# Kernel tuning notes

Measured on AMD Instinct MI355X. Metric: run time of the kernel, lower is better.

## Reference

```python
import jax, jax.numpy as jnp
import numpy as np

B, N, D, NS, H, ITERS = 16, 2048, 128, 8, 128, 3
EPS = 1e-8


def _ln(x, g, b):
    m = jnp.mean(x, -1, keepdims=True)
    v = jnp.mean((x - m) ** 2, -1, keepdims=True)
    return (x - m) * jax.lax.rsqrt(v + 1e-5) * g + b


def _gru(x, h, Wih, Whh, bih, bhh):
    # PyTorch GRUCell math
    gi = x @ Wih.T + bih
    gh = h @ Whh.T + bhh
    ir, iz, inn = jnp.split(gi, 3, -1)
    hr, hz, hn = jnp.split(gh, 3, -1)
    r = jax.nn.sigmoid(ir + hr)
    z = jax.nn.sigmoid(iz + hz)
    n = jnp.tanh(inn + r * hn)
    return (1.0 - z) * n + z * h


def setup_inputs() -> dict:
    key = jax.random.key(0)
    ks = jax.random.split(key, 16)

    def lin(k, out_d, in_d):
        lim = 1.0 / np.sqrt(in_d)
        return jax.random.uniform(k, (out_d, in_d), jnp.float32, -lim, lim)

    return {
        "inputs": jax.random.normal(ks[0], (B, N, D), jnp.float32),
        "init_noise": jax.random.normal(ks[1], (B, NS, 2 * D), jnp.float32),
        "slots_mu": jax.random.normal(ks[2], (1, 1, 2 * D), jnp.float32),
        "slots_logsigma": jax.random.normal(ks[3], (1, 1, 2 * D), jnp.float32) * 0.08,  # ~xavier scale
        "Wq": lin(ks[4], D, D),
        "Wk": lin(ks[5], D, D),
        "gru_Wih": lin(ks[6], 3 * D, D),
        "gru_Whh": lin(ks[7], 3 * D, D),
        "gru_bih": jnp.zeros((3 * D,), jnp.float32),
        "gru_bhh": jnp.zeros((3 * D,), jnp.float32),
        "mlp_mu_W1": lin(ks[8], H, D),
        "mlp_mu_b1": jnp.zeros((H,), jnp.float32),
        "mlp_mu_W2": lin(ks[9], D, H),
        "mlp_mu_b2": jnp.zeros((D,), jnp.float32),
        "ln_in_g": jnp.ones((D,), jnp.float32),
        "ln_in_b": jnp.zeros((D,), jnp.float32),
        "ln_slots_g": jnp.ones((2 * D,), jnp.float32),
        "ln_slots_b": jnp.zeros((2 * D,), jnp.float32),
        "ln_mu_g": jnp.ones((D,), jnp.float32),
        "ln_mu_b": jnp.zeros((D,), jnp.float32),
        "mlp_out_W1": lin(ks[10], 2 * H, 2 * D),
        "mlp_out_b1": jnp.zeros((2 * H,), jnp.float32),
        "mlp_out_W2": lin(ks[11], D, 2 * H),
        "mlp_out_b2": jnp.zeros((D,), jnp.float32),
    }


def _forward(inputs, init_noise, slots_mu, slots_logsigma, Wq, Wk,
             gru_Wih, gru_Whh, gru_bih, gru_bhh,
             mlp_mu_W1, mlp_mu_b1, mlp_mu_W2, mlp_mu_b2,
             ln_in_g, ln_in_b, ln_slots_g, ln_slots_b, ln_mu_g, ln_mu_b,
             mlp_out_W1, mlp_out_b1, mlp_out_W2, mlp_out_b2):
    x = _ln(inputs, ln_in_g, ln_in_b)                      # (B,N,D)
    k = x @ Wk.T
    v = k                                                  # original uses to_k for both k and v
    slots = slots_mu + jnp.exp(slots_logsigma) * init_noise  # (B,NS,2D)
    pi_cl = jnp.full((B, NS, 1), 1.0 / NS, inputs.dtype)

    def step(slots, pi_cl):
        s = _ln(slots, ln_slots_g, ln_slots_b)
        mu_s, ls_s = jnp.split(s, 2, -1)                   # (B,NS,D) each
        q_mu = mu_s @ Wq.T
        q_ls = ls_s @ Wq.T
        inv_var = jnp.exp(-2.0 * q_ls)                     # 1 / exp(q_logsigma)^2
        diff = k[:, None, :, :] - q_mu[:, :, None, :]      # (B,NS,N,D)
        dots = jnp.einsum('bind,bid->bin', diff * diff, inv_var)
        dots_exp = (jnp.exp(-dots) + EPS) * pi_cl          # (B,NS,N)
        gammas = dots_exp / dots_exp.sum(1, keepdims=True)
        attn = gammas / gammas.sum(-1, keepdims=True)
        upd = jnp.einsum('bjd,bij->bid', v, attn)          # (B,NS,D)
        upd = _gru(upd.reshape(-1, D), mu_s.reshape(-1, D),
                   gru_Wih, gru_Whh, gru_bih, gru_bhh).reshape(B, NS, D)
        h = _ln(upd, ln_mu_g, ln_mu_b)
        upd = upd + (jax.nn.relu(h @ mlp_mu_W1.T + mlp_mu_b1) @ mlp_mu_W2.T + mlp_mu_b2)
        diff2 = v[:, None, :, :] - upd[:, :, None, :]      # (B,NS,N,D)
        upd_ls = 0.5 * jnp.log(jnp.einsum('bind,bin->bid', diff2 * diff2 + EPS, attn))
        slots_new = jnp.concatenate([upd, upd_ls], -1)
        pi_new = gammas.sum(-1, keepdims=True)
        pi_new = pi_new / pi_new.shape[2]                  # shape[2]==1: faithful no-op from original
        return slots_new, pi_new

    for _ in range(ITERS):
        slots, pi_cl = step(slots, pi_cl)
    slots, pi_cl = step(jax.lax.stop_gradient(slots), pi_cl)
    h = jax.nn.relu(slots @ mlp_out_W1.T + mlp_out_b1)
    return h @ mlp_out_W2.T + mlp_out_b2                   # (B,NS,D)


def reference(inputs, init_noise, slots_mu, slots_logsigma, Wq, Wk,
              gru_Wih, gru_Whh, gru_bih, gru_bhh,
              mlp_mu_W1, mlp_mu_b1, mlp_mu_W2, mlp_mu_b2,
              ln_in_g, ln_in_b, ln_slots_g, ln_slots_b, ln_mu_g, ln_mu_b,
              mlp_out_W1, mlp_out_b1, mlp_out_W2, mlp_out_b2):
    return _forward(inputs, init_noise, slots_mu, slots_logsigma, Wq, Wk,
                    gru_Wih, gru_Whh, gru_bih, gru_bhh,
                    mlp_mu_W1, mlp_mu_b1, mlp_mu_W2, mlp_mu_b2,
                    ln_in_g, ln_in_b, ln_slots_g, ln_slots_b, ln_mu_g, ln_mu_b,
                    mlp_out_W1, mlp_out_b1, mlp_out_W2, mlp_out_b2)
```

## Files before the change

### kernel.cpp

```cpp
#include <hip/hip_runtime.h>

#define EPS_ 1e-8f

constexpr int OFF_K     = 0;
constexpr int OFF_WQT   = 4194304;
constexpr int OFF_WKT   = OFF_WQT  + 16384;
constexpr int OFF_WIHT  = OFF_WKT  + 16384;
constexpr int OFF_WHHT  = OFF_WIHT + 49152;
constexpr int OFF_WM1T  = OFF_WHHT + 49152;
constexpr int OFF_WM2T  = OFF_WM1T + 16384;
constexpr int OFF_WO1T  = OFF_WM2T + 16384;
constexpr int OFF_WO2T  = OFF_WO1T + 65536;
constexpr int OFF_SLOTS = OFF_WO2T + 32768;
constexpr int OFF_PI    = OFF_SLOTS+ 32768;
constexpr int OFF_MUS   = OFF_PI   + 128;
constexpr int OFF_QMU   = OFF_MUS  + 16384;
constexpr int OFF_IVAR  = OFF_QMU  + 16384;
constexpr int OFF_UN    = OFF_IVAR + 16384;
constexpr int OFF_S2    = OFF_UN   + 262144;
constexpr int OFF_DEN   = OFF_S2   + 262144;

__global__ __launch_bounds__(256) void init_kernel(
    const float* __restrict__ Wq,  const float* __restrict__ Wk,
    const float* __restrict__ Wih, const float* __restrict__ Whh,
    const float* __restrict__ Wm1, const float* __restrict__ Wm2,
    const float* __restrict__ Wo1, const float* __restrict__ Wo2,
    const float* __restrict__ smu, const float* __restrict__ sls,
    const float* __restrict__ noise, float* __restrict__ ws) {
  int idx = blockIdx.x * 256 + threadIdx.x;
  if (idx < 16384) { int j = idx >> 7, d = idx & 127; ws[OFF_WQT + d*128 + j] = Wq[idx]; return; }
  idx -= 16384;
  if (idx < 16384) { int j = idx >> 7, d = idx & 127; ws[OFF_WKT + d*128 + j] = Wk[idx]; return; }
  idx -= 16384;
  if (idx < 49152) { int j = idx >> 7, d = idx & 127; ws[OFF_WIHT + d*384 + j] = Wih[idx]; return; }
  idx -= 49152;
  if (idx < 49152) { int j = idx >> 7, d = idx & 127; ws[OFF_WHHT + d*384 + j] = Whh[idx]; return; }
  idx -= 49152;
  if (idx < 16384) { int j = idx >> 7, d = idx & 127; ws[OFF_WM1T + d*128 + j] = Wm1[idx]; return; }
  idx -= 16384;
  if (idx < 16384) { int j = idx >> 7, d = idx & 127; ws[OFF_WM2T + d*128 + j] = Wm2[idx]; return; }
  idx -= 16384;
  if (idx < 65536) { int j = idx >> 8, d = idx & 255; ws[OFF_WO1T + d*256 + j] = Wo1[idx]; return; }
  idx -= 65536;
  if (idx < 32768) { int j = idx >> 8, m = idx & 255; ws[OFF_WO2T + m*128 + j] = Wo2[idx]; return; }
  idx -= 32768;
  if (idx < 32768) { int c = idx & 255; ws[OFF_SLOTS + idx] = smu[c] + expf(sls[c]) * noise[idx]; return; }
  idx -= 32768;
  if (idx < 128) { ws[OFF_PI + idx] = 0.125f; }
}

__global__ __launch_bounds__(256) void k_kernel(
    const float* __restrict__ xin, const float* __restrict__ g, const float* __restrict__ bb,
    const float* __restrict__ WkT, float* __restrict__ kout) {
  __shared__ float xs[16][128];
  __shared__ float2 red[16][16];
  __shared__ float mrow[16], srow[16];
  int t = threadIdx.x;
  int base = blockIdx.x * 2048;
  const float4* in4 = (const float4*)(xin + base);
  for (int f = t; f < 512; f += 256) {
    float4 v = in4[f];
    *(float4*)&xs[f >> 5][(f & 31) * 4] = v;
  }
  __syncthreads();
  {
    int row = t >> 4, l = t & 15;
    float s = 0.f, ss = 0.f;
    #pragma unroll
    for (int d = 0; d < 128; d += 16) { float v = xs[row][d + l]; s += v; ss = fmaf(v, v, ss); }
    red[row][l] = make_float2(s, ss);
  }
  __syncthreads();
  if (t < 16) {
    float s = 0.f, ss = 0.f;
    #pragma unroll
    for (int l = 0; l < 16; ++l) { float2 p = red[t][l]; s += p.x; ss += p.y; }
    float m = s * (1.0f/128.0f);
    float var = ss * (1.0f/128.0f) - m * m;
    mrow[t] = m;
    srow[t] = rsqrtf(var + 1e-5f);
  }
  __syncthreads();
  for (int f = t; f < 2048; f += 256) {
    int row = f >> 7, d = f & 127;
    xs[row][d] = (xs[row][d] - mrow[row]) * srow[row] * g[d] + bb[d];
  }
  __syncthreads();
  int j = t & 127, half = t >> 7;
  float acc[8] = {0,0,0,0,0,0,0,0};
  const int r0 = half * 8;
  #pragma unroll 4
  for (int d = 0; d < 128; ++d) {
    float w = WkT[d * 128 + j];
    #pragma unroll
    for (int r = 0; r < 8; ++r) acc[r] = fmaf(w, xs[r0 + r][d], acc[r]);
  }
  #pragma unroll
  for (int r = 0; r < 8; ++r) kout[base + (r0 + r) * 128 + j] = acc[r];
}

__global__ __launch_bounds__(256) void s1_kernel(
    const float* __restrict__ slots, const float* __restrict__ g, const float* __restrict__ bb,
    const float* __restrict__ WqT, float* __restrict__ mus, float* __restrict__ qmu,
    float* __restrict__ ivar) {
  __shared__ float sl[256];
  __shared__ float2 wr[4];
  int t = threadIdx.x, bi = blockIdx.x;
  float v = slots[bi * 256 + t];
  float s = v, ss = v * v;
  #pragma unroll
  for (int o = 32; o > 0; o >>= 1) { s += __shfl_down(s, o); ss += __shfl_down(ss, o); }
  if ((t & 63) == 0) wr[t >> 6] = make_float2(s, ss);
  __syncthreads();
  float fs  = wr[0].x + wr[1].x + wr[2].x + wr[3].x;
  float fss = wr[0].y + wr[1].y + wr[2].y + wr[3].y;
  float m   = fs * (1.0f/256.0f);
  float var = fss * (1.0f/256.0f) - m * m;
  float isr = rsqrtf(var + 1e-5f);
  float sn  = (v - m) * isr * g[t] + bb[t];
  sl[t] = sn;
  __syncthreads();
  if (t < 128) {
    float acc = 0.f;
    #pragma unroll 4
    for (int d = 0; d < 128; ++d) acc = fmaf(sl[d], WqT[d * 128 + t], acc);
    qmu[bi * 128 + t] = acc;
    mus[bi * 128 + t] = sn;
  } else {
    int jj = t - 128;
    float acc = 0.f;
    #pragma unroll 4
    for (int d = 0; d < 128; ++d) acc = fmaf(sl[128 + d], WqT[d * 128 + jj], acc);
    ivar[bi * 128 + jj] = expf(-2.0f * acc);
  }
}

__global__ __launch_bounds__(1024) void s2_kernel(
    const float* __restrict__ kmat, const float* __restrict__ qmu,
    const float* __restrict__ ivar, const float* __restrict__ pi,
    float* __restrict__ wun, float* __restrict__ ws2, float* __restrict__ wden) {
  __shared__ float kc[128][132];
  __shared__ float qs[8 * 132];
  __shared__ float ivs[8 * 132];
  __shared__ float es[8 * 132];
  __shared__ float gam[128 * 12];
  __shared__ float recip[128];
  __shared__ float pis[8];
  __shared__ float pU[4][8][128];
  __shared__ float pS[4][8][128];
  __shared__ float pd[8][8];
  int t = threadIdx.x;
  int chunk = blockIdx.x, b = blockIdx.y;
  if (t < 8) pis[t] = pi[b * 8 + t];
  { int ii = t >> 7, dd = t & 127;
    qs[ii * 132 + dd]  = qmu[b * 1024 + t];
    ivs[ii * 132 + dd] = ivar[b * 1024 + t]; }
  const float4* k4 = (const float4*)(kmat + (b * 2048 + chunk * 128) * 128);
  for (int f = t; f < 4096; f += 1024)
    *(float4*)&kc[f >> 5][(f & 31) * 4] = k4[f];
  __syncthreads();
  if (t < 512) {
    int gsl = t & 7, n0 = (t >> 3) << 1;
    float acc0 = 0.f, acc1 = 0.f;
    const float* qrow = qs + gsl * 132;
    const float* irow = ivs + gsl * 132;
    const float* k0r  = &kc[n0][0];
    const float* k1r  = &kc[n0 + 1][0];
    #pragma unroll 4
    for (int dq = 0; dq < 32; ++dq) {
      float4 qv = *(const float4*)(qrow + dq * 4);
      float4 iv = *(const float4*)(irow + dq * 4);
      float4 k0 = *(const float4*)(k0r + dq * 4);
      float4 k1 = *(const float4*)(k1r + dq * 4);
      float e;
      e = k0.x - qv.x; acc0 = fmaf(e * e, iv.x, acc0);
      e = k0.y - qv.y; acc0 = fmaf(e * e, iv.y, acc0);
      e = k0.z - qv.z; acc0 = fmaf(e * e, iv.z, acc0);
      e = k0.w - qv.w; acc0 = fmaf(e * e, iv.w, acc0);
      e = k1.x - qv.x; acc1 = fmaf(e * e, iv.x, acc1);
      e = k1.y - qv.y; acc1 = fmaf(e * e, iv.y, acc1);
      e = k1.z - qv.z; acc1 = fmaf(e * e, iv.z, acc1);
      e = k1.w - qv.w; acc1 = fmaf(e * e, iv.w, acc1);
    }
    es[gsl * 132 + n0]     = (expf(-acc0) + EPS_) * pis[gsl];
    es[gsl * 132 + n0 + 1] = (expf(-acc1) + EPS_) * pis[gsl];
  }
  __syncthreads();
  if (t < 128) {
    float ssum = 0.f;
    #pragma unroll
    for (int g2 = 0; g2 < 8; ++g2) ssum += es[g2 * 132 + t];
    recip[t] = 1.0f / ssum;
  }
  __syncthreads();
  { int ii = t >> 7, n = t & 127;
    gam[n * 12 + ii] = es[ii * 132 + n] * recip[n]; }
  __syncthreads();
  if (t < 512) {
    int grp = t >> 7, dd = t & 127;
    float un[8] = {0,0,0,0,0,0,0,0};
    float s2[8] = {0,0,0,0,0,0,0,0};
    #pragma unroll 2
    for (int n = grp * 32; n < grp * 32 + 32; ++n) {
      float kk  = kc[n][dd];
      float kk2 = kk * kk;
      float4 g0 = *(const float4*)&gam[n * 12];
      float4 g1 = *(const float4*)&gam[n * 12 + 4];
      un[0] = fmaf(g0.x, kk, un[0]); s2[0] = fmaf(g0.x, kk2, s2[0]);
      un[1] = fmaf(g0.y, kk, un[1]); s2[1] = fmaf(g0.y, kk2, s2[1]);
      un[2] = fmaf(g0.z, kk, un[2]); s2[2] = fmaf(g0.z, kk2, s2[2]);
      un[3] = fmaf(g0.w, kk, un[3]); s2[3] = fmaf(g0.w, kk2, s2[3]);
      un[4] = fmaf(g1.x, kk, un[4]); s2[4] = fmaf(g1.x, kk2, s2[4]);
      un[5] = fmaf(g1.y, kk, un[5]); s2[5] = fmaf(g1.y, kk2, s2[5]);
      un[6] = fmaf(g1.z, kk, un[6]); s2[6] = fmaf(g1.z, kk2, s2[6]);
      un[7] = fmaf(g1.w, kk, un[7]); s2[7] = fmaf(g1.w, kk2, s2[7]);
    }
    #pragma unroll
    for (int ii = 0; ii < 8; ++ii) { pU[grp][ii][dd] = un[ii]; pS[grp][ii][dd] = s2[ii]; }
  } else if (t < 576) {
    int ii = (t - 512) & 7, sub = (t - 512) >> 3;
    float dsum = 0.f;
    for (int n = sub * 16; n < sub * 16 + 16; ++n) dsum += gam[n * 12 + ii];
    pd[sub][ii] = dsum;
  }
  __syncthreads();
  { int ii = t >> 7, dd = t & 127;
    int pbase = ((b * 16 + chunk) * 8 + ii) * 128 + dd;
    wun[pbase] = pU[0][ii][dd] + pU[1][ii][dd] + pU[2][ii][dd] + pU[3][ii][dd];
    ws2[pbase] = pS[0][ii][dd] + pS[1][ii][dd] + pS[2][ii][dd] + pS[3][ii][dd]; }
  if (t < 8) {
    float s = 0.f;
    #pragma unroll
    for (int sub = 0; sub < 8; ++sub) s += pd[sub][t];
    wden[(b * 16 + chunk) * 8 + t] = s;
  }
}

__global__ __launch_bounds__(512) void s3_kernel(
    const float* __restrict__ wun, const float* __restrict__ ws2, const float* __restrict__ wden,
    const float* __restrict__ WihT, const float* __restrict__ WhhT,
    const float* __restrict__ bih,  const float* __restrict__ bhh,
    const float* __restrict__ Wm1T, const float* __restrict__ bm1,
    const float* __restrict__ Wm2T, const float* __restrict__ bm2,
    const float* __restrict__ gmu,  const float* __restrict__ bmu,
    float* __restrict__ slots, float* __restrict__ pi,
    int do_s1,
    const float* __restrict__ gs, const float* __restrict__ bs,
    const float* __restrict__ WqT,
    float* __restrict__ mus, float* __restrict__ qmu, float* __restrict__ ivar,
    const float* __restrict__ Wo1T, const float* __restrict__ bo1,
    const float* __restrict__ Wo2T, const float* __restrict__ bo2,
    float* __restrict__ out) {
  int t = threadIdx.x, bi = blockIdx.x;
  int d = t & 127, q = t >> 7;
  int b = bi >> 3, i = bi & 7;
  __shared__ float redU[4][128], redS[4][128];
  __shared__ float dred[16];
  __shared__ float xs[128], hs[128];
  __shared__ float gacc[4][6][128];
  __shared__ float ga[6][128];
  __shared__ float grus[128], hl[128], m1s[128];
  __shared__ float macc[4][128];
  __shared__ float2 wr2[2];
  __shared__ float uarr[256];
  float unp = 0.f, s2p = 0.f;
  #pragma unroll
  for (int c = q * 4; c < q * 4 + 4; ++c) {
    int po = ((b * 16 + c) * 8 + i) * 128 + d;
    unp += wun[po]; s2p += ws2[po];
  }
  redU[q][d] = unp; redS[q][d] = s2p;
  if (t < 16) dred[t] = wden[(b * 16 + t) * 8 + i];
  if (q == 1) hs[d] = mus[bi * 128 + d];
  __syncthreads();
  float den = 0.f;
  #pragma unroll
  for (int c = 0; c < 16; ++c) den += dred[c];
  float un  = redU[0][d] + redU[1][d] + redU[2][d] + redU[3][d];
  float s2v = redS[0][d] + redS[1][d] + redS[2][d] + redS[3][d];
  if (q == 0) xs[d] = un / den;
  __syncthreads();
  {
    float a0 = 0, a1 = 0, a2 = 0, a3 = 0, a4 = 0, a5 = 0;
    #pragma unroll 4
    for (int dd = q * 32; dd < q * 32 + 32; ++dd) {
      float xv = xs[dd], hv = hs[dd];
      const float* wi = &WihT[dd * 384 + d];
      const float* wh = &WhhT[dd * 384 + d];
      a0 = fmaf(xv, wi[0],   a0);
      a1 = fmaf(xv, wi[128], a1);
      a2 = fmaf(xv, wi[256], a2);
      a3 = fmaf(hv, wh[0],   a3);
      a4 = fmaf(hv, wh[128], a4);
      a5 = fmaf(hv, wh[256], a5);
    }
    gacc[q][0][d] = a0; gacc[q][1][d] = a1; gacc[q][2][d] = a2;
    gacc[q][3][d] = a3; gacc[q][4][d] = a4; gacc[q][5][d] = a5;
  }
  __syncthreads();
  for (int f = t; f < 768; f += 512) {
    int j = f >> 7, dd = f & 127;
    ga[j][dd] = gacc[0][j][dd] + gacc[1][j][dd] + gacc[2][j][dd] + gacc[3][j][dd];
  }
  __syncthreads();
  float gru = 0.f;
  if (q == 0) {
    float ir = ga[0][d] + bih[d], iz = ga[1][d] + bih[128 + d], inn = ga[2][d] + bih[256 + d];
    float hr = ga[3][d] + bhh[d], hz = ga[4][d] + bhh[128 + d], hn  = ga[5][d] + bhh[256 + d];
    float r  = 1.0f / (1.0f + expf(-(ir + hr)));
    float z  = 1.0f / (1.0f + expf(-(iz + hz)));
    float nn = tanhf(inn + r * hn);
    gru = (1.0f - z) * nn + z * hs[d];
    grus[d] = gru;
    float s = gru, ssq = gru * gru;
    #pragma unroll
    for (int o = 32; o > 0; o >>= 1) { s += __shfl_down(s, o); ssq += __shfl_down(ssq, o); }
    if ((d & 63) == 0) wr2[d >> 6] = make_float2(s, ssq);
  }
  __syncthreads();
  if (q == 0) {
    float fs = wr2[0].x + wr2[1].x, fss = wr2[0].y + wr2[1].y;
    float mean = fs * (1.0f/128.0f);
    float var  = fss * (1.0f/128.0f) - mean * mean;
    hl[d] = (gru - mean) * rsqrtf(var + 1e-5f) * gmu[d] + bmu[d];
  }
  __syncthreads();
  {
    float m1p = 0.f;
    #pragma unroll 4
    for (int dd = q * 32; dd < q * 32 + 32; ++dd)
      m1p = fmaf(hl[dd], Wm1T[dd * 128 + d], m1p);
    macc[q][d] = m1p;
  }
  __syncthreads();
  if (q == 0) m1s[d] = fmaxf(macc[0][d] + macc[1][d] + macc[2][d] + macc[3][d] + bm1[d], 0.f);
  __syncthreads();
  {
    float m2p = 0.f;
    #pragma unroll 4
    for (int dd = q * 32; dd < q * 32 + 32; ++dd)
      m2p = fmaf(m1s[dd], Wm2T[dd * 128 + d], m2p);
    macc[q][d] = m2p;
  }
  __syncthreads();
  if (q == 0) {
    float u = grus[d] + macc[0][d] + macc[1][d] + macc[2][d] + macc[3][d] + bm2[d];
    float val = (s2v - 2.0f * u * un + u * u * den) / den;
    float ls = 0.5f * logf(fmaxf(val, 0.0f) + EPS_);
    slots[bi * 256 + d]       = u;
    slots[bi * 256 + 128 + d] = ls;
    uarr[d] = u; uarr[128 + d] = ls;
    if (d == 0) pi[bi] = den;
  }
  __syncthreads();
  if (do_s1) {
    __shared__ float2 wr4[4];
    __shared__ float sln[256];
    __shared__ float qacc[2][2][128];
    if (t < 256) {
      float v = uarr[t];
      float s = v, ssq = v * v;
      #pragma unroll
      for (int o = 32; o > 0; o >>= 1) { s += __shfl_down(s, o); ssq += __shfl_down(ssq, o); }
      if ((t & 63) == 0) wr4[t >> 6] = make_float2(s, ssq);
    }
    __syncthreads();
    if (t < 256) {
      float fs  = wr4[0].x + wr4[1].x + wr4[2].x + wr4[3].x;
      float fss = wr4[0].y + wr4[1].y + wr4[2].y + wr4[3].y;
      float m   = fs * (1.0f/256.0f);
      float var = fss * (1.0f/256.0f) - m * m;
      sln[t] = (uarr[t] - m) * rsqrtf(var + 1e-5f) * gs[t] + bs[t];
    }
    __syncthreads();
    {
      int h2 = t >> 8, qq = (t >> 7) & 1, d2 = t & 127;
      const float* src = sln + h2 * 128;
      float acc = 0.f;
      #pragma unroll 4
      for (int dd = qq * 64; dd < qq * 64 + 64; ++dd)
        acc = fmaf(src[dd], WqT[dd * 128 + d2], acc);
      qacc[h2][qq][d2] = acc;
    }
    __syncthreads();
    if (t < 128) {
      qmu[bi * 128 + t] = qacc[0][0][t] + qacc[0][1][t];
      mus[bi * 128 + t] = sln[t];
    } else if (t < 256) {
      int dd2 = t - 128;
      ivar[bi * 128 + dd2] = expf(-2.0f * (qacc[1][0][dd2] + qacc[1][1][dd2]));
    }
  } else {
    __shared__ float oacc[2][256];
    __shared__ float hh[256];
    {
      int o = t & 255, qq = t >> 8;
      float acc = 0.f;
      #pragma unroll 4
      for (int dd = qq * 128; dd < qq * 128 + 128; ++dd)
        acc = fmaf(uarr[dd], Wo1T[dd * 256 + o], acc);
      oacc[qq][o] = acc;
    }
    __syncthreads();
    if (t < 256) hh[t] = fmaxf(oacc[0][t] + oacc[1][t] + bo1[t], 0.f);
    __syncthreads();
    {
      int o2 = t & 127, q4 = t >> 7;
      float acc2 = 0.f;
      #pragma unroll 4
      for (int dd = q4 * 64; dd < q4 * 64 + 64; ++dd)
        acc2 = fmaf(hh[dd], Wo2T[dd * 128 + o2], acc2);
      macc[q4][o2] = acc2;
    }
    __syncthreads();
    if (t < 128) out[bi * 128 + t] = macc[0][t] + macc[1][t] + macc[2][t] + macc[3][t] + bo2[t];
  }
}

extern "C" void kernel_launch(void* const* d_in, const int* in_sizes, int n_in,
                              void* d_out, int out_size, void* d_ws, size_t ws_size,
                              hipStream_t stream) {
  const float* inputs = (const float*)d_in[0];
  const float* noise  = (const float*)d_in[1];
  const float* smu    = (const float*)d_in[2];
  const float* sls    = (const float*)d_in[3];
  const float* Wq     = (const float*)d_in[4];
  const float* Wk     = (const float*)d_in[5];
  const float* Wih    = (const float*)d_in[6];
  const float* Whh    = (const float*)d_in[7];
  const float* bih    = (const float*)d_in[8];
  const float* bhh    = (const float*)d_in[9];
  const float* Wm1    = (const float*)d_in[10];
  const float* bm1    = (const float*)d_in[11];
  const float* Wm2    = (const float*)d_in[12];
  const float* bm2    = (const float*)d_in[13];
  const float* gin    = (const float*)d_in[14];
  const float* bin    = (const float*)d_in[15];
  const float* gsl    = (const float*)d_in[16];
  const float* bsl    = (const float*)d_in[17];
  const float* gmu    = (const float*)d_in[18];
  const float* bmu    = (const float*)d_in[19];
  const float* Wo1    = (const float*)d_in[20];
  const float* bo1    = (const float*)d_in[21];
  const float* Wo2    = (const float*)d_in[22];
  const float* bo2    = (const float*)d_in[23];

  float* ws    = (float*)d_ws;
  float* kbuf  = ws + OFF_K;
  float* WqT   = ws + OFF_WQT;
  float* WkT   = ws + OFF_WKT;
  float* WihT  = ws + OFF_WIHT;
  float* WhhT  = ws + OFF_WHHT;
  float* Wm1T  = ws + OFF_WM1T;
  float* Wm2T  = ws + OFF_WM2T;
  float* Wo1T  = ws + OFF_WO1T;
  float* Wo2T  = ws + OFF_WO2T;
  float* slots = ws + OFF_SLOTS;
  float* pibuf = ws + OFF_PI;
  float* mus   = ws + OFF_MUS;
  float* qmu   = ws + OFF_QMU;
  float* ivar  = ws + OFF_IVAR;
  float* wun   = ws + OFF_UN;
  float* ws2   = ws + OFF_S2;
  float* wden  = ws + OFF_DEN;

  hipLaunchKernelGGL(init_kernel, dim3(1153), dim3(256), 0, stream,
                     Wq, Wk, Wih, Whh, Wm1, Wm2, Wo1, Wo2, smu, sls, noise, ws);
  hipLaunchKernelGGL(k_kernel, dim3(2048), dim3(256), 0, stream,
                     inputs, gin, bin, WkT, kbuf);
  hipLaunchKernelGGL(s1_kernel, dim3(128), dim3(256), 0, stream,
                     slots, gsl, bsl, WqT, mus, qmu, ivar);
  for (int s = 0; s < 4; ++s) {
    hipLaunchKernelGGL(s2_kernel, dim3(16, 16), dim3(1024), 0, stream,
                       kbuf, qmu, ivar, pibuf, wun, ws2, wden);
    hipLaunchKernelGGL(s3_kernel, dim3(128), dim3(512), 0, stream,
                       wun, ws2, wden, WihT, WhhT, bih, bhh,
                       Wm1T, bm1, Wm2T, bm2, gmu, bmu, slots, pibuf,
                       (s < 3) ? 1 : 0, gsl, bsl, WqT, mus, qmu, ivar,
                       Wo1T, bo1, Wo2T, bo2, (float*)d_out);
  }
}
```

Baseline: 168.4 us.

## Retile key projection with shared-memory weights and rework s2 distance-stage mapping

The key-projection kernel now processes 64 rows per block, stages the full WkT matrix in shared memory, and has each thread compute 32 outputs for one row with vectorized float4 stores. This cuts the grid from 2048 to 512 blocks and is meant to reduce repeated global weight reads. In s2, the K chunk is stored with an XOR-swizzled float4 layout to avoid bank conflicts. All 1024 threads now compute the distance scores, split over two halves of the feature dimension and combined afterward, which costs an extra shared buffer and barrier. Shared-memory use per block rises sharply in both kernels, which may reduce occupancy.

Measured after the change: 181.4 us. 1.08x slower.

```diff
diff --git a/kernel.cpp b/kernel.cpp
--- a/kernel.cpp
+++ b/kernel.cpp
@@ -52,51 +52,68 @@
 __global__ __launch_bounds__(256) void k_kernel(
     const float* __restrict__ xin, const float* __restrict__ g, const float* __restrict__ bb,
     const float* __restrict__ WkT, float* __restrict__ kout) {
-  __shared__ float xs[16][128];
-  __shared__ float2 red[16][16];
-  __shared__ float mrow[16], srow[16];
+  __shared__ float xs[64][129];
+  __shared__ float4 wt4[128 * 32];
+  __shared__ float2 red2[64][4];
+  __shared__ float mrow[64], srow[64];
   int t = threadIdx.x;
-  int base = blockIdx.x * 2048;
+  long long base = (long long)blockIdx.x * 64 * 128;
   const float4* in4 = (const float4*)(xin + base);
-  for (int f = t; f < 512; f += 256) {
+  for (int f = t; f < 2048; f += 256) {
     float4 v = in4[f];
-    *(float4*)&xs[f >> 5][(f & 31) * 4] = v;
-  }
-  __syncthreads();
-  {
-    int row = t >> 4, l = t & 15;
+    int r = f >> 5, gg = (f & 31) * 4;
+    xs[r][gg] = v.x; xs[r][gg + 1] = v.y; xs[r][gg + 2] = v.z; xs[r][gg + 3] = v.w;
+  }
+  const float4* w4 = (const float4*)WkT;
+  for (int f = t; f < 4096; f += 256) wt4[f] = w4[f];
+  __syncthreads();
+  {
+    int r = t >> 2, qq = t & 3;
     float s = 0.f, ss = 0.f;
-    #pragma unroll
-    for (int d = 0; d < 128; d += 16) { float v = xs[row][d + l]; s += v; ss = fmaf(v, v, ss); }
-    red[row][l] = make_float2(s, ss);
-  }
-  __syncthreads();
-  if (t < 16) {
+    #pragma unroll 8
+    for (int u = 0; u < 32; ++u) { float v = xs[r][qq * 32 + u]; s += v; ss = fmaf(v, v, ss); }
+    red2[r][qq] = make_float2(s, ss);
+  }
+  __syncthreads();
+  if (t < 64) {
     float s = 0.f, ss = 0.f;
     #pragma unroll
-    for (int l = 0; l < 16; ++l) { float2 p = red[t][l]; s += p.x; ss += p.y; }
-    float m = s * (1.0f/128.0f);
-    float var = ss * (1.0f/128.0f) - m * m;
-    mrow[t] = m;
-    srow[t] = rsqrtf(var + 1e-5f);
-  }
-  __syncthreads();
-  for (int f = t; f < 2048; f += 256) {
-    int row = f >> 7, d = f & 127;
-    xs[row][d] = (xs[row][d] - mrow[row]) * srow[row] * g[d] + bb[d];
-  }
-  __syncthreads();
-  int j = t & 127, half = t >> 7;
-  float acc[8] = {0,0,0,0,0,0,0,0};
-  const int r0 = half * 8;
-  #pragma unroll 4
+    for (int qq = 0; qq < 4; ++qq) { float2 p = red2[t][qq]; s += p.x; ss += p.y; }
+    float m = s * (1.0f / 128.0f);
+    float var = ss * (1.0f / 128.0f) - m * m;
+    mrow[t] = m; srow[t] = rsqrtf(var + 1e-5f);
+  }
+  __syncthreads();
+  {
+    int r = t >> 2, qq = t & 3;
+    float m = mrow[r], is = srow[r];
+    #pragma unroll 8
+    for (int u = 0; u < 32; ++u) {
+      int d = qq * 32 + u;
+      xs[r][d] = (xs[r][d] - m) * is * g[d] + bb[d];
+    }
+  }
+  __syncthreads();
+  int r = t & 63, jg = t >> 6;
+  float acc[32];
+  #pragma unroll
+  for (int i = 0; i < 32; ++i) acc[i] = 0.f;
+  #pragma unroll 2
   for (int d = 0; d < 128; ++d) {
-    float w = WkT[d * 128 + j];
-    #pragma unroll
-    for (int r = 0; r < 8; ++r) acc[r] = fmaf(w, xs[r0 + r][d], acc[r]);
-  }
+    float xv = xs[r][d];
+    #pragma unroll
+    for (int i = 0; i < 8; ++i) {
+      float4 wv = wt4[d * 32 + jg * 8 + i];
+      acc[i * 4 + 0] = fmaf(xv, wv.x, acc[i * 4 + 0]);
+      acc[i * 4 + 1] = fmaf(xv, wv.y, acc[i * 4 + 1]);
+      acc[i * 4 + 2] = fmaf(xv, wv.z, acc[i * 4 + 2]);
+      acc[i * 4 + 3] = fmaf(xv, wv.w, acc[i * 4 + 3]);
+    }
+  }
+  float* orow = kout + base + (long long)r * 128 + jg * 32;
   #pragma unroll
-  for (int r = 0; r < 8; ++r) kout[base + (r0 + r) * 128 + j] = acc[r];
+  for (int i = 0; i < 8; ++i)
+    *(float4*)(orow + i * 4) = make_float4(acc[i*4], acc[i*4+1], acc[i*4+2], acc[i*4+3]);
 }
 
 __global__ __launch_bounds__(256) void s1_kernel(
@@ -139,11 +156,12 @@
     const float* __restrict__ kmat, const float* __restrict__ qmu,
     const float* __restrict__ ivar, const float* __restrict__ pi,
     float* __restrict__ wun, float* __restrict__ ws2, float* __restrict__ wden) {
-  __shared__ float kc[128][132];
-  __shared__ float qs[8 * 132];
-  __shared__ float ivs[8 * 132];
-  __shared__ float es[8 * 132];
-  __shared__ float gam[128 * 12];
+  __shared__ float4 kc4[128 * 32];
+  __shared__ float4 qs4[8 * 32];
+  __shared__ float4 ivs4[8 * 32];
+  __shared__ float esp[2][8][128];
+  __shared__ float es_[8][128];
+  __shared__ float gam_[128][8];
   __shared__ float recip[128];
   __shared__ float pis[8];
   __shared__ float pU[4][8][128];
@@ -152,60 +170,72 @@
   int t = threadIdx.x;
   int chunk = blockIdx.x, b = blockIdx.y;
   if (t < 8) pis[t] = pi[b * 8 + t];
-  { int ii = t >> 7, dd = t & 127;
-    qs[ii * 132 + dd]  = qmu[b * 1024 + t];
-    ivs[ii * 132 + dd] = ivar[b * 1024 + t]; }
-  const float4* k4 = (const float4*)(kmat + (b * 2048 + chunk * 128) * 128);
-  for (int f = t; f < 4096; f += 1024)
-    *(float4*)&kc[f >> 5][(f & 31) * 4] = k4[f];
-  __syncthreads();
-  if (t < 512) {
-    int gsl = t & 7, n0 = (t >> 3) << 1;
+  if (t < 256) {
+    qs4[t]  = ((const float4*)qmu)[b * 256 + t];
+    ivs4[t] = ((const float4*)ivar)[b * 256 + t];
+  }
+  const float4* k4 = (const float4*)(kmat + (long long)(b * 2048 + chunk * 128) * 128);
+  for (int f = t; f < 4096; f += 1024) {
+    int n = f >> 5, gg = f & 31;
+    kc4[n * 32 + (gg ^ (n & 31))] = k4[f];
+  }
+  __syncthreads();
+  {
+    int w = t >> 6, lane = t & 63;
+    int sp = w & 3, nh = (w >> 2) & 1, dh = w >> 3;
+    int s0 = sp * 2, s1 = s0 + 1;
+    int n = nh * 64 + lane;
+    int nx = n & 31;
+    const float4* kr = kc4 + n * 32;
     float acc0 = 0.f, acc1 = 0.f;
-    const float* qrow = qs + gsl * 132;
-    const float* irow = ivs + gsl * 132;
-    const float* k0r  = &kc[n0][0];
-    const float* k1r  = &kc[n0 + 1][0];
-    #pragma unroll 4
-    for (int dq = 0; dq < 32; ++dq) {
-      float4 qv = *(const float4*)(qrow + dq * 4);
-      float4 iv = *(const float4*)(irow + dq * 4);
-      float4 k0 = *(const float4*)(k0r + dq * 4);
-      float4 k1 = *(const float4*)(k1r + dq * 4);
+    #pragma unroll
+    for (int gi = 0; gi < 16; ++gi) {
+      int gg = dh * 16 + gi;
+      float4 kv = kr[gg ^ nx];
+      float4 q0 = qs4[s0 * 32 + gg], i0 = ivs4[s0 * 32 + gg];
+      float4 q1 = qs4[s1 * 32 + gg], i1 = ivs4[s1 * 32 + gg];
       float e;
-      e = k0.x - qv.x; acc0 = fmaf(e * e, iv.x, acc0);
-      e = k0.y - qv.y; acc0 = fmaf(e * e, iv.y, acc0);
-      e = k0.z - qv.z; acc0 = fmaf(e * e, iv.z, acc0);
-      e = k0.w - qv.w; acc0 = fmaf(e * e, iv.w, acc0);
-      e = k1.x - qv.x; acc1 = fmaf(e * e, iv.x, acc1);
-      e = k1.y - qv.y; acc1 = fmaf(e * e, iv.y, acc1);
-      e = k1.z - qv.z; acc1 = fmaf(e * e, iv.z, acc1);
-      e = k1.w - qv.w; acc1 = fmaf(e * e, iv.w, acc1);
-    }
-    es[gsl * 132 + n0]     = (expf(-acc0) + EPS_) * pis[gsl];
-    es[gsl * 132 + n0 + 1] = (expf(-acc1) + EPS_) * pis[gsl];
+      e = kv.x - q0.x; acc0 = fmaf(e * e, i0.x, acc0);
+      e = kv.y - q0.y; acc0 = fmaf(e * e, i0.y, acc0);
+      e = kv.z - q0.z; acc0 = fmaf(e * e, i0.z, acc0);
+      e = kv.w - q0.w; acc0 = fmaf(e * e, i0.w, acc0);
+      e = kv.x - q1.x; acc1 = fmaf(e * e, i1.x, acc1);
+      e = kv.y - q1.y; acc1 = fmaf(e * e, i1.y, acc1);
+      e = kv.z - q1.z; acc1 = fmaf(e * e, i1.z, acc1);
+      e = kv.w - q1.w; acc1 = fmaf(e * e, i1.w, acc1);
+    }
+    esp[dh][s0][n] = acc0;
+    esp[dh][s1][n] = acc1;
+  }
+  __syncthreads();
+  {
+    int s = t >> 7, n = t & 127;
+    float dots = esp[0][s][n] + esp[1][s][n];
+    es_[s][n] = (expf(-dots) + EPS_) * pis[s];
   }
   __syncthreads();
   if (t < 128) {
     float ssum = 0.f;
     #pragma unroll
-    for (int g2 = 0; g2 < 8; ++g2) ssum += es[g2 * 132 + t];
+    for (int s = 0; s < 8; ++s) ssum += es_[s][t];
     recip[t] = 1.0f / ssum;
   }
   __syncthreads();
-  { int ii = t >> 7, n = t & 127;
-    gam[n * 12 + ii] = es[ii * 132 + n] * recip[n]; }
+  { int s = t >> 7, n = t & 127;
+    gam_[n][s] = es_[s][n] * recip[n]; }
   __syncthreads();
   if (t < 512) {
     int grp = t >> 7, dd = t & 127;
+    const float* kcf = (const float*)kc4;
     float un[8] = {0,0,0,0,0,0,0,0};
     float s2[8] = {0,0,0,0,0,0,0,0};
+    int gbase = dd >> 2, elem = dd & 3;
     #pragma unroll 2
     for (int n = grp * 32; n < grp * 32 + 32; ++n) {
-      float kk  = kc[n][dd];
+      float kk  = kcf[n * 128 + 4 * (gbase ^ (n & 31)) + elem];
       float kk2 = kk * kk;
-      float4 g0 = *(const float4*)&gam[n * 12];
-      float4 g1 = *(const float4*)&gam[n * 12 + 4];
+      float4 g0 = *(const float4*)&gam_[n][0];
+      float4 g1 = *(const float4*)&gam_[n][4];
       un[0] = fmaf(g0.x, kk, un[0]); s2[0] = fmaf(g0.x, kk2, s2[0]);
       un[1] = fmaf(g0.y, kk, un[1]); s2[1] = fmaf(g0.y, kk2, s2[1]);
       un[2] = fmaf(g0.z, kk, un[2]); s2[2] = fmaf(g0.z, kk2, s2[2]);
@@ -216,18 +246,18 @@
       un[7] = fmaf(g1.w, kk, un[7]); s2[7] = fmaf(g1.w, kk2, s2[7]);
     }
     #pragma unroll
-    for (int ii = 0; ii < 8; ++ii) { pU[grp][ii][dd] = un[ii]; pS[grp][ii][dd] = s2[ii]; }
+    for (int i = 0; i < 8; ++i) { pU[grp][i][dd] = un[i]; pS[grp][i][dd] = s2[i]; }
   } else if (t < 576) {
-    int ii = (t - 512) & 7, sub = (t - 512) >> 3;
+    int i = (t - 512) & 7, sub = (t - 512) >> 3;
     float dsum = 0.f;
-    for (int n = sub * 16; n < sub * 16 + 16; ++n) dsum += gam[n * 12 + ii];
-    pd[sub][ii] = dsum;
-  }
-  __syncthreads();
-  { int ii = t >> 7, dd = t & 127;
-    int pbase = ((b * 16 + chunk) * 8 + ii) * 128 + dd;
-    wun[pbase] = pU[0][ii][dd] + pU[1][ii][dd] + pU[2][ii][dd] + pU[3][ii][dd];
-    ws2[pbase] = pS[0][ii][dd] + pS[1][ii][dd] + pS[2][ii][dd] + pS[3][ii][dd]; }
+    for (int n = sub * 16; n < sub * 16 + 16; ++n) dsum += gam_[n][i];
+    pd[sub][i] = dsum;
+  }
+  __syncthreads();
+  { int i = t >> 7, dd = t & 127;
+    int pbase = ((b * 16 + chunk) * 8 + i) * 128 + dd;
+    wun[pbase] = pU[0][i][dd] + pU[1][i][dd] + pU[2][i][dd] + pU[3][i][dd];
+    ws2[pbase] = pS[0][i][dd] + pS[1][i][dd] + pS[2][i][dd] + pS[3][i][dd]; }
   if (t < 8) {
     float s = 0.f;
     #pragma unroll
@@ -466,7 +496,7 @@
 
   hipLaunchKernelGGL(init_kernel, dim3(1153), dim3(256), 0, stream,
                      Wq, Wk, Wih, Whh, Wm1, Wm2, Wo1, Wo2, smu, sls, noise, ws);
-  hipLaunchKernelGGL(k_kernel, dim3(2048), dim3(256), 0, stream,
+  hipLaunchKernelGGL(k_kernel, dim3(512), dim3(256), 0, stream,
                      inputs, gin, bin, WkT, kbuf);
   hipLaunchKernelGGL(s1_kernel, dim3(128), dim3(256), 0, stream,
                      slots, gsl, bsl, WqT, mus, qmu, ivar);
```

## Expand Gaussian distance algebraically and retile k and s2 kernels

Applied to the files above, without the earlier changes.

The Mahalanobis-style distance sum((k-q)^2*ivar) is expanded into k^2*ivar + k*(-2q*ivar) + const. The per-slot coefficients and the constant are precomputed in s1 and s3, so s2 streams k straight from global memory without staging a padded shared tile. s2 moves to 512-thread blocks over 64-token chunks (32 chunks per batch), and s3 reduces 32 partials per slot instead of 16. k_kernel now processes 32 rows per block, keeps the layernorm in registers and writes a swizzled transposed shared tile for float4 reads. The expansion risks cancellation error when k is close to q.

Result: slower. 174.0 us (+3.4%).

```diff
diff --git a/kernel.cpp b/kernel.cpp
--- a/kernel.cpp
+++ b/kernel.cpp
@@ -14,11 +14,12 @@
 constexpr int OFF_SLOTS = OFF_WO2T + 32768;
 constexpr int OFF_PI    = OFF_SLOTS+ 32768;
 constexpr int OFF_MUS   = OFF_PI   + 128;
-constexpr int OFF_QMU   = OFF_MUS  + 16384;
-constexpr int OFF_IVAR  = OFF_QMU  + 16384;
-constexpr int OFF_UN    = OFF_IVAR + 16384;
-constexpr int OFF_S2    = OFF_UN   + 262144;
-constexpr int OFF_DEN   = OFF_S2   + 262144;
+constexpr int OFF_WA    = OFF_MUS  + 16384;
+constexpr int OFF_WB    = OFF_WA   + 16384;
+constexpr int OFF_UN    = OFF_WB   + 16384;
+constexpr int OFF_S2    = OFF_UN   + 524288;
+constexpr int OFF_DEN   = OFF_S2   + 524288;
+constexpr int OFF_CZ    = OFF_DEN  + 4096;
 
 __global__ __launch_bounds__(256) void init_kernel(
     const float* __restrict__ Wq,  const float* __restrict__ Wk,
@@ -52,59 +53,81 @@
 __global__ __launch_bounds__(256) void k_kernel(
     const float* __restrict__ xin, const float* __restrict__ g, const float* __restrict__ bb,
     const float* __restrict__ WkT, float* __restrict__ kout) {
-  __shared__ float xs[16][128];
-  __shared__ float2 red[16][16];
-  __shared__ float mrow[16], srow[16];
+  __shared__ float xsT[128][32];
+  __shared__ float2 red[32][8];
+  __shared__ float mrow[32], srow[32];
   int t = threadIdx.x;
-  int base = blockIdx.x * 2048;
-  const float4* in4 = (const float4*)(xin + base);
-  for (int f = t; f < 512; f += 256) {
-    float4 v = in4[f];
-    *(float4*)&xs[f >> 5][(f & 31) * 4] = v;
-  }
-  __syncthreads();
-  {
-    int row = t >> 4, l = t & 15;
+  long long base = (long long)blockIdx.x * 32 * 128;
+  int row = t >> 3, cg = t & 7;
+  const float4* src = (const float4*)(xin + base + row * 128 + cg * 16);
+  float4 v0 = src[0], v1 = src[1], v2 = src[2], v3 = src[3];
+  const float4* g4p = (const float4*)(g + cg * 16);
+  const float4* b4p = (const float4*)(bb + cg * 16);
+  float4 g0 = g4p[0], g1 = g4p[1], g2 = g4p[2], g3 = g4p[3];
+  float4 bv0 = b4p[0], bv1 = b4p[1], bv2 = b4p[2], bv3 = b4p[3];
+  float vals[16];
+  *(float4*)&vals[0]  = v0; *(float4*)&vals[4]  = v1;
+  *(float4*)&vals[8]  = v2; *(float4*)&vals[12] = v3;
+  float gl[16], bl[16];
+  *(float4*)&gl[0] = g0; *(float4*)&gl[4] = g1; *(float4*)&gl[8] = g2; *(float4*)&gl[12] = g3;
+  *(float4*)&bl[0] = bv0; *(float4*)&bl[4] = bv1; *(float4*)&bl[8] = bv2; *(float4*)&bl[12] = bv3;
+  {
     float s = 0.f, ss = 0.f;
     #pragma unroll
-    for (int d = 0; d < 128; d += 16) { float v = xs[row][d + l]; s += v; ss = fmaf(v, v, ss); }
-    red[row][l] = make_float2(s, ss);
-  }
-  __syncthreads();
-  if (t < 16) {
+    for (int i = 0; i < 16; ++i) { float v = vals[i]; s += v; ss = fmaf(v, v, ss); }
+    red[row][cg] = make_float2(s, ss);
+  }
+  __syncthreads();
+  if (t < 32) {
     float s = 0.f, ss = 0.f;
     #pragma unroll
-    for (int l = 0; l < 16; ++l) { float2 p = red[t][l]; s += p.x; ss += p.y; }
-    float m = s * (1.0f/128.0f);
-    float var = ss * (1.0f/128.0f) - m * m;
-    mrow[t] = m;
-    srow[t] = rsqrtf(var + 1e-5f);
-  }
-  __syncthreads();
-  for (int f = t; f < 2048; f += 256) {
-    int row = f >> 7, d = f & 127;
-    xs[row][d] = (xs[row][d] - mrow[row]) * srow[row] * g[d] + bb[d];
-  }
-  __syncthreads();
-  int j = t & 127, half = t >> 7;
-  float acc[8] = {0,0,0,0,0,0,0,0};
-  const int r0 = half * 8;
+    for (int c = 0; c < 8; ++c) { float2 p = red[t][c]; s += p.x; ss += p.y; }
+    float m = s * (1.0f / 128.0f);
+    float var = ss * (1.0f / 128.0f) - m * m;
+    mrow[t] = m; srow[t] = rsqrtf(var + 1e-5f);
+  }
+  __syncthreads();
+  {
+    float m = mrow[row], is = srow[row];
+    #pragma unroll
+    for (int i = 0; i < 16; ++i) {
+      int d = cg * 16 + i;
+      int rs = row ^ (((d >> 2) & 7) << 2);
+      xsT[d][rs] = (vals[i] - m) * is * gl[i] + bl[i];
+    }
+  }
+  __syncthreads();
+  int j = t & 127, rh = t >> 7;
+  int r0 = rh * 16;
+  float acc[16];
+  #pragma unroll
+  for (int i = 0; i < 16; ++i) acc[i] = 0.f;
   #pragma unroll 4
   for (int d = 0; d < 128; ++d) {
-    float w = WkT[d * 128 + j];
-    #pragma unroll
-    for (int r = 0; r < 8; ++r) acc[r] = fmaf(w, xs[r0 + r][d], acc[r]);
+    float wv = WkT[d * 128 + j];
+    int X = ((d >> 2) & 7) << 2;
+    #pragma unroll
+    for (int gi = 0; gi < 4; ++gi) {
+      int off = (r0 + gi * 4) ^ X;
+      float4 xv = *(const float4*)&xsT[d][off];
+      acc[gi * 4 + 0] = fmaf(xv.x, wv, acc[gi * 4 + 0]);
+      acc[gi * 4 + 1] = fmaf(xv.y, wv, acc[gi * 4 + 1]);
+      acc[gi * 4 + 2] = fmaf(xv.z, wv, acc[gi * 4 + 2]);
+      acc[gi * 4 + 3] = fmaf(xv.w, wv, acc[gi * 4 + 3]);
+    }
   }
   #pragma unroll
-  for (int r = 0; r < 8; ++r) kout[base + (r0 + r) * 128 + j] = acc[r];
+  for (int i = 0; i < 16; ++i) kout[base + (long long)(r0 + i) * 128 + j] = acc[i];
 }
 
 __global__ __launch_bounds__(256) void s1_kernel(
     const float* __restrict__ slots, const float* __restrict__ g, const float* __restrict__ bb,
-    const float* __restrict__ WqT, float* __restrict__ mus, float* __restrict__ qmu,
-    float* __restrict__ ivar) {
+    const float* __restrict__ WqT, float* __restrict__ mus,
+    float* __restrict__ wA, float* __restrict__ wB, float* __restrict__ cz) {
   __shared__ float sl[256];
   __shared__ float2 wr[4];
+  __shared__ float qs_l[128], ivs_l[128];
+  __shared__ float wrC[4];
   int t = threadIdx.x, bi = blockIdx.x;
   float v = slots[bi * 256 + t];
   float s = v, ss = v * v;
@@ -124,115 +147,128 @@
     float acc = 0.f;
     #pragma unroll 4
     for (int d = 0; d < 128; ++d) acc = fmaf(sl[d], WqT[d * 128 + t], acc);
-    qmu[bi * 128 + t] = acc;
+    qs_l[t] = acc;
     mus[bi * 128 + t] = sn;
   } else {
     int jj = t - 128;
     float acc = 0.f;
     #pragma unroll 4
     for (int d = 0; d < 128; ++d) acc = fmaf(sl[128 + d], WqT[d * 128 + jj], acc);
-    ivar[bi * 128 + jj] = expf(-2.0f * acc);
-  }
+    ivs_l[jj] = expf(-2.0f * acc);
+  }
+  __syncthreads();
+  float cp = 0.f;
+  if (t < 128) {
+    float iv = ivs_l[t], q = qs_l[t];
+    wA[bi * 128 + t] = iv;
+    wB[bi * 128 + t] = -2.0f * q * iv;
+    cp = q * q * iv;
+  }
+  #pragma unroll
+  for (int o = 32; o > 0; o >>= 1) cp += __shfl_down(cp, o);
+  if ((t & 63) == 0) wrC[t >> 6] = cp;
+  __syncthreads();
+  if (t == 0) cz[bi] = wrC[0] + wrC[1];
 }
 
-__global__ __launch_bounds__(1024) void s2_kernel(
-    const float* __restrict__ kmat, const float* __restrict__ qmu,
-    const float* __restrict__ ivar, const float* __restrict__ pi,
+__global__ __launch_bounds__(512) void s2_kernel(
+    const float* __restrict__ kmat, const float* __restrict__ wA,
+    const float* __restrict__ wB,  const float* __restrict__ cz,
+    const float* __restrict__ pi,
     float* __restrict__ wun, float* __restrict__ ws2, float* __restrict__ wden) {
-  __shared__ float kc[128][132];
-  __shared__ float qs[8 * 132];
-  __shared__ float ivs[8 * 132];
-  __shared__ float es[8 * 132];
-  __shared__ float gam[128 * 12];
-  __shared__ float recip[128];
-  __shared__ float pis[8];
-  __shared__ float pU[4][8][128];
-  __shared__ float pS[4][8][128];
+  __shared__ float pdots[8][64][8];
+  __shared__ float es[64][8];
+  __shared__ float recip[64];
+  __shared__ float gT[8][72];
   __shared__ float pd[8][8];
+  __shared__ float pisl[8], czl[8];
   int t = threadIdx.x;
   int chunk = blockIdx.x, b = blockIdx.y;
-  if (t < 8) pis[t] = pi[b * 8 + t];
-  { int ii = t >> 7, dd = t & 127;
-    qs[ii * 132 + dd]  = qmu[b * 1024 + t];
-    ivs[ii * 132 + dd] = ivar[b * 1024 + t]; }
-  const float4* k4 = (const float4*)(kmat + (b * 2048 + chunk * 128) * 128);
-  for (int f = t; f < 4096; f += 1024)
-    *(float4*)&kc[f >> 5][(f & 31) * 4] = k4[f];
-  __syncthreads();
-  if (t < 512) {
-    int gsl = t & 7, n0 = (t >> 3) << 1;
-    float acc0 = 0.f, acc1 = 0.f;
-    const float* qrow = qs + gsl * 132;
-    const float* irow = ivs + gsl * 132;
-    const float* k0r  = &kc[n0][0];
-    const float* k1r  = &kc[n0 + 1][0];
-    #pragma unroll 4
-    for (int dq = 0; dq < 32; ++dq) {
-      float4 qv = *(const float4*)(qrow + dq * 4);
-      float4 iv = *(const float4*)(irow + dq * 4);
-      float4 k0 = *(const float4*)(k0r + dq * 4);
-      float4 k1 = *(const float4*)(k1r + dq * 4);
-      float e;
-      e = k0.x - qv.x; acc0 = fmaf(e * e, iv.x, acc0);
-      e = k0.y - qv.y; acc0 = fmaf(e * e, iv.y, acc0);
-      e = k0.z - qv.z; acc0 = fmaf(e * e, iv.z, acc0);
-      e = k0.w - qv.w; acc0 = fmaf(e * e, iv.w, acc0);
-      e = k1.x - qv.x; acc1 = fmaf(e * e, iv.x, acc1);
-      e = k1.y - qv.y; acc1 = fmaf(e * e, iv.y, acc1);
-      e = k1.z - qv.z; acc1 = fmaf(e * e, iv.z, acc1);
-      e = k1.w - qv.w; acc1 = fmaf(e * e, iv.w, acc1);
-    }
-    es[gsl * 132 + n0]     = (expf(-acc0) + EPS_) * pis[gsl];
-    es[gsl * 132 + n0 + 1] = (expf(-acc1) + EPS_) * pis[gsl];
-  }
-  __syncthreads();
-  if (t < 128) {
+  if (t < 8) { pisl[t] = pi[b * 8 + t]; czl[t] = cz[b * 8 + t]; }
+  {
+    int n = t & 63, w = t >> 6;
+    const float4* kr4 = (const float4*)(kmat + (long long)((b * 2048 + chunk * 64 + n) * 128 + w * 16));
+    const float4* wa4 = (const float4*)(wA + b * 1024);
+    const float4* wb4 = (const float4*)(wB + b * 1024);
+    float acc[8] = {0,0,0,0,0,0,0,0};
+    #pragma unroll
+    for (int dq = 0; dq < 4; ++dq) {
+      float4 kv = kr4[dq];
+      float xx = kv.x * kv.x, yy = kv.y * kv.y, zz = kv.z * kv.z, ww = kv.w * kv.w;
+      #pragma unroll
+      for (int s = 0; s < 8; ++s) {
+        float4 a4 = wa4[s * 32 + w * 4 + dq];
+        float4 b4 = wb4[s * 32 + w * 4 + dq];
+        float ac = acc[s];
+        ac = fmaf(xx, a4.x, ac); ac = fmaf(kv.x, b4.x, ac);
+        ac = fmaf(yy, a4.y, ac); ac = fmaf(kv.y, b4.y, ac);
+        ac = fmaf(zz, a4.z, ac); ac = fmaf(kv.z, b4.z, ac);
+        ac = fmaf(ww, a4.w, ac); ac = fmaf(kv.w, b4.w, ac);
+        acc[s] = ac;
+      }
+    }
+    *(float4*)&pdots[w][n][0] = make_float4(acc[0], acc[1], acc[2], acc[3]);
+    *(float4*)&pdots[w][n][4] = make_float4(acc[4], acc[5], acc[6], acc[7]);
+  }
+  __syncthreads();
+  float e;
+  {
+    int n2 = t >> 3, s = t & 7;
+    float dots = czl[s];
+    #pragma unroll
+    for (int w = 0; w < 8; ++w) dots += pdots[w][n2][s];
+    e = (expf(-dots) + EPS_) * pisl[s];
+    es[n2][s] = e;
+  }
+  __syncthreads();
+  if (t < 64) {
     float ssum = 0.f;
     #pragma unroll
-    for (int g2 = 0; g2 < 8; ++g2) ssum += es[g2 * 132 + t];
+    for (int s = 0; s < 8; ++s) ssum += es[t][s];
     recip[t] = 1.0f / ssum;
   }
   __syncthreads();
-  { int ii = t >> 7, n = t & 127;
-    gam[n * 12 + ii] = es[ii * 132 + n] * recip[n]; }
-  __syncthreads();
-  if (t < 512) {
-    int grp = t >> 7, dd = t & 127;
-    float un[8] = {0,0,0,0,0,0,0,0};
-    float s2[8] = {0,0,0,0,0,0,0,0};
+  {
+    int n2 = t >> 3, s = t & 7;
+    float gam = e * recip[n2];
+    gT[s][n2] = gam;
+    float p = gam;
+    p += __shfl_down(p, 8); p += __shfl_down(p, 16); p += __shfl_down(p, 32);
+    if ((t & 63) < 8) pd[t >> 6][t & 7] = p;
+  }
+  __syncthreads();
+  if (t < 8) {
+    float sden = 0.f;
+    #pragma unroll
+    for (int w = 0; w < 8; ++w) sden += pd[w][t];
+    wden[(b * 32 + chunk) * 8 + t] = sden;
+  }
+  {
+    int d = t & 127, sh = t >> 7;
+    int s0 = sh * 2, s1 = s0 + 1;
+    const float* kcol = kmat + (long long)(b * 2048 + chunk * 64) * 128 + d;
+    float u0 = 0.f, u1 = 0.f, q0 = 0.f, q1 = 0.f;
     #pragma unroll 2
-    for (int n = grp * 32; n < grp * 32 + 32; ++n) {
-      float kk  = kc[n][dd];
-      float kk2 = kk * kk;
-      float4 g0 = *(const float4*)&gam[n * 12];
-      float4 g1 = *(const float4*)&gam[n * 12 + 4];
-      un[0] = fmaf(g0.x, kk, un[0]); s2[0] = fmaf(g0.x, kk2, s2[0]);
-      un[1] = fmaf(g0.y, kk, un[1]); s2[1] = fmaf(g0.y, kk2, s2[1]);
-      un[2] = fmaf(g0.z, kk, un[2]); s2[2] = fmaf(g0.z, kk2, s2[2]);
-      un[3] = fmaf(g0.w, kk, un[3]); s2[3] = fmaf(g0.w, kk2, s2[3]);
-      un[4] = fmaf(g1.x, kk, un[4]); s2[4] = fmaf(g1.x, kk2, s2[4]);
-      un[5] = fmaf(g1.y, kk, un[5]); s2[5] = fmaf(g1.y, kk2, s2[5]);
-      un[6] = fmaf(g1.z, kk, un[6]); s2[6] = fmaf(g1.z, kk2, s2[6]);
-      un[7] = fmaf(g1.w, kk, un[7]); s2[7] = fmaf(g1.w, kk2, s2[7]);
-    }
-    #pragma unroll
-    for (int ii = 0; ii < 8; ++ii) { pU[grp][ii][dd] = un[ii]; pS[grp][ii][dd] = s2[ii]; }
-  } else if (t < 576) {
-    int ii = (t - 512) & 7, sub = (t - 512) >> 3;
-    float dsum = 0.f;
-    for (int n = sub * 16; n < sub * 16 + 16; ++n) dsum += gam[n * 12 + ii];
-    pd[sub][ii] = dsum;
-  }
-  __syncthreads();
-  { int ii = t >> 7, dd = t & 127;
-    int pbase = ((b * 16 + chunk) * 8 + ii) * 128 + dd;
-    wun[pbase] = pU[0][ii][dd] + pU[1][ii][dd] + pU[2][ii][dd] + pU[3][ii][dd];
-    ws2[pbase] = pS[0][ii][dd] + pS[1][ii][dd] + pS[2][ii][dd] + pS[3][ii][dd]; }
-  if (t < 8) {
-    float s = 0.f;
-    #pragma unroll
-    for (int sub = 0; sub < 8; ++sub) s += pd[sub][t];
-    wden[(b * 16 + chunk) * 8 + t] = s;
+    for (int n3 = 0; n3 < 64; n3 += 4) {
+      float4 ga = *(const float4*)&gT[s0][n3];
+      float4 gb = *(const float4*)&gT[s1][n3];
+      float k0 = kcol[(n3 + 0) * 128];
+      float k1 = kcol[(n3 + 1) * 128];
+      float k2 = kcol[(n3 + 2) * 128];
+      float k3 = kcol[(n3 + 3) * 128];
+      float k0s = k0 * k0, k1s = k1 * k1, k2s = k2 * k2, k3s = k3 * k3;
+      u0 = fmaf(ga.x, k0, u0); q0 = fmaf(ga.x, k0s, q0);
+      u1 = fmaf(gb.x, k0, u1); q1 = fmaf(gb.x, k0s, q1);
+      u0 = fmaf(ga.y, k1, u0); q0 = fmaf(ga.y, k1s, q0);
+      u1 = fmaf(gb.y, k1, u1); q1 = fmaf(gb.y, k1s, q1);
+      u0 = fmaf(ga.z, k2, u0); q0 = fmaf(ga.z, k2s, q0);
+      u1 = fmaf(gb.z, k2, u1); q1 = fmaf(gb.z, k2s, q1);
+      u0 = fmaf(ga.w, k3, u0); q0 = fmaf(ga.w, k3s, q0);
+      u1 = fmaf(gb.w, k3, u1); q1 = fmaf(gb.w, k3s, q1);
+    }
+    int pb = ((b * 32 + chunk) * 8) * 128 + d;
+    wun[pb + s0 * 128] = u0; wun[pb + s1 * 128] = u1;
+    ws2[pb + s0 * 128] = q0; ws2[pb + s1 * 128] = q1;
   }
 }
 
@@ -247,7 +283,8 @@
     int do_s1,
     const float* __restrict__ gs, const float* __restrict__ bs,
     const float* __restrict__ WqT,
-    float* __restrict__ mus, float* __restrict__ qmu, float* __restrict__ ivar,
+    float* __restrict__ mus, float* __restrict__ wAo, float* __restrict__ wBo,
+    float* __restrict__ czo,
     const float* __restrict__ Wo1T, const float* __restrict__ bo1,
     const float* __restrict__ Wo2T, const float* __restrict__ bo2,
     float* __restrict__ out) {
@@ -255,7 +292,7 @@
   int d = t & 127, q = t >> 7;
   int b = bi >> 3, i = bi & 7;
   __shared__ float redU[4][128], redS[4][128];
-  __shared__ float dred[16];
+  __shared__ float dred[32];
   __shared__ float xs[128], hs[128];
   __shared__ float gacc[4][6][128];
   __shared__ float ga[6][128];
@@ -265,17 +302,17 @@
   __shared__ float uarr[256];
   float unp = 0.f, s2p = 0.f;
   #pragma unroll
-  for (int c = q * 4; c < q * 4 + 4; ++c) {
-    int po = ((b * 16 + c) * 8 + i) * 128 + d;
+  for (int c = q * 8; c < q * 8 + 8; ++c) {
+    int po = ((b * 32 + c) * 8 + i) * 128 + d;
     unp += wun[po]; s2p += ws2[po];
   }
   redU[q][d] = unp; redS[q][d] = s2p;
-  if (t < 16) dred[t] = wden[(b * 16 + t) * 8 + i];
+  if (t < 32) dred[t] = wden[(b * 32 + t) * 8 + i];
   if (q == 1) hs[d] = mus[bi * 128 + d];
   __syncthreads();
   float den = 0.f;
   #pragma unroll
-  for (int c = 0; c < 16; ++c) den += dred[c];
+  for (int c = 0; c < 32; ++c) den += dred[c];
   float un  = redU[0][d] + redU[1][d] + redU[2][d] + redU[3][d];
   float s2v = redS[0][d] + redS[1][d] + redS[2][d] + redS[3][d];
   if (q == 0) xs[d] = un / den;
@@ -357,6 +394,8 @@
     __shared__ float2 wr4[4];
     __shared__ float sln[256];
     __shared__ float qacc[2][2][128];
+    __shared__ float qs_l[128], ivs_l[128];
+    __shared__ float wrC[8];
     if (t < 256) {
       float v = uarr[t];
       float s = v, ssq = v * v;
@@ -384,12 +423,25 @@
     }
     __syncthreads();
     if (t < 128) {
-      qmu[bi * 128 + t] = qacc[0][0][t] + qacc[0][1][t];
+      qs_l[t] = qacc[0][0][t] + qacc[0][1][t];
       mus[bi * 128 + t] = sln[t];
     } else if (t < 256) {
       int dd2 = t - 128;
-      ivar[bi * 128 + dd2] = expf(-2.0f * (qacc[1][0][dd2] + qacc[1][1][dd2]));
-    }
+      ivs_l[dd2] = expf(-2.0f * (qacc[1][0][dd2] + qacc[1][1][dd2]));
+    }
+    __syncthreads();
+    float cp = 0.f;
+    if (t < 128) {
+      float iv = ivs_l[t], qv = qs_l[t];
+      wAo[bi * 128 + t] = iv;
+      wBo[bi * 128 + t] = -2.0f * qv * iv;
+      cp = qv * qv * iv;
+    }
+    #pragma unroll
+    for (int o = 32; o > 0; o >>= 1) cp += __shfl_down(cp, o);
+    if ((t & 63) == 0) wrC[t >> 6] = cp;
+    __syncthreads();
+    if (t == 0) czo[bi] = wrC[0] + wrC[1];
   } else {
     __shared__ float oacc[2][256];
     __shared__ float hh[256];
@@ -458,25 +510,26 @@
   float* slots = ws + OFF_SLOTS;
   float* pibuf = ws + OFF_PI;
   float* mus   = ws + OFF_MUS;
-  float* qmu   = ws + OFF_QMU;
-  float* ivar  = ws + OFF_IVAR;
+  float* wA    = ws + OFF_WA;
+  float* wB    = ws + OFF_WB;
   float* wun   = ws + OFF_UN;
   float* ws2   = ws + OFF_S2;
   float* wden  = ws + OFF_DEN;
+  float* czb   = ws + OFF_CZ;
 
   hipLaunchKernelGGL(init_kernel, dim3(1153), dim3(256), 0, stream,
                      Wq, Wk, Wih, Whh, Wm1, Wm2, Wo1, Wo2, smu, sls, noise, ws);
-  hipLaunchKernelGGL(k_kernel, dim3(2048), dim3(256), 0, stream,
+  hipLaunchKernelGGL(k_kernel, dim3(1024), dim3(256), 0, stream,
                      inputs, gin, bin, WkT, kbuf);
   hipLaunchKernelGGL(s1_kernel, dim3(128), dim3(256), 0, stream,
-                     slots, gsl, bsl, WqT, mus, qmu, ivar);
+                     slots, gsl, bsl, WqT, mus, wA, wB, czb);
   for (int s = 0; s < 4; ++s) {
-    hipLaunchKernelGGL(s2_kernel, dim3(16, 16), dim3(1024), 0, stream,
-                       kbuf, qmu, ivar, pibuf, wun, ws2, wden);
+    hipLaunchKernelGGL(s2_kernel, dim3(32, 16), dim3(512), 0, stream,
+                       kbuf, wA, wB, czb, pibuf, wun, ws2, wden);
     hipLaunchKernelGGL(s3_kernel, dim3(128), dim3(512), 0, stream,
                        wun, ws2, wden, WihT, WhhT, bih, bhh,
                        Wm1T, bm1, Wm2T, bm2, gmu, bmu, slots, pibuf,
-                       (s < 3) ? 1 : 0, gsl, bsl, WqT, mus, qmu, ivar,
+                       (s < 3) ? 1 : 0, gsl, bsl, WqT, mus, wA, wB, czb,
                        Wo1T, bo1, Wo2T, bo2, (float*)d_out);
   }
 }
```
